# Kernel optimization log

Measured on AMD Instinct MI355X. Metric: run time of the kernel, lower is better.

## Reference

```python
import jax, jax.numpy as jnp
import numpy as np

EPS = 1e-5
N_HEADS = 16
D_NOPE = 128
D_ROPE = 64
D_QK = D_NOPE + D_ROPE  # 192
D_V = 128
KV_RANK = 512
SCALE = D_QK ** -0.5


def rms_norm(x, w, eps=EPS):
    return x * jax.lax.rsqrt(jnp.mean(x * x, axis=-1, keepdims=True) + eps) * w


def apply_rope(x, c, s):
    # x: [..., D_ROPE], c/s broadcastable [..., D_ROPE//2]; half-split rotation
    x0, x1 = x[..., : D_ROPE // 2], x[..., D_ROPE // 2 :]
    return jnp.concatenate([x0 * c - x1 * s, x0 * s + x1 * c], axis=-1)


def setup_inputs() -> dict:
    key = jax.random.key(0)
    ks = jax.random.split(key, 8)
    B, S, H_DIM = 2, 2048, 2048
    Q_RANK = 1536
    w = lambda k, shp: jax.random.normal(k, shp, dtype=jnp.float32) * 0.02
    # real RoPE tables: [max_seq, D_ROPE//2]
    inv_freq = 1.0 / (10000.0 ** (np.arange(0, D_ROPE, 2, dtype=np.float32) / D_ROPE))
    ang = np.arange(S, dtype=np.float32)[:, None] * inv_freq[None, :]
    return {
        "x": jax.random.normal(ks[0], (B, S, H_DIM), dtype=jnp.float32),
        "positions": jnp.arange(S, dtype=jnp.int64),
        "Wqa": w(ks[1], (H_DIM, Q_RANK)),
        "g_qa": jnp.ones((Q_RANK,), jnp.float32),
        "Wqb": w(ks[2], (Q_RANK, N_HEADS * D_QK)),
        "Wkva": w(ks[3], (H_DIM, KV_RANK + D_ROPE)),
        "g_kva": jnp.ones((KV_RANK,), jnp.float32),
        "Wkvb": w(ks[4], (KV_RANK, N_HEADS * (D_NOPE + D_V))),
        "Wo": w(ks[5], (N_HEADS * D_V, H_DIM)),
        "cos": jnp.asarray(np.cos(ang)),
        "sin": jnp.asarray(np.sin(ang)),
    }


def reference(x, positions, Wqa, g_qa, Wqb, Wkva, g_kva, Wkvb, Wo, cos, sin):
    B, S, _ = x.shape
    # Q path: low-rank down, RMSNorm, up
    q = rms_norm(x @ Wqa, g_qa) @ Wqb  # [B,S,H*D_QK]
    q = q.reshape(B, S, N_HEADS, D_QK)
    q_nope, q_rope = q[..., :D_NOPE], q[..., D_NOPE:]
    c = cos[positions]  # [S, D_ROPE//2]
    s = sin[positions]
    q_rope = apply_rope(q_rope, c[None, :, None, :], s[None, :, None, :])
    # KV path: joint down-proj, split latent / rope-key
    kv_a = x @ Wkva  # [B,S,KV_RANK+D_ROPE]
    kv_latent = rms_norm(kv_a[..., :KV_RANK], g_kva)
    k_rope = apply_rope(kv_a[..., KV_RANK:], c[None, :, :], s[None, :, :])  # [B,S,D_ROPE]
    # up-project latent to per-head k_nope and v
    kv_b = (kv_latent @ Wkvb).reshape(B, S, N_HEADS, D_NOPE + D_V)
    k_nope, v = kv_b[..., :D_NOPE], kv_b[..., D_NOPE:]
    k = jnp.concatenate(
        [k_nope, jnp.broadcast_to(k_rope[:, :, None, :], (B, S, N_HEADS, D_ROPE))], axis=-1
    )  # [B,S,H,D_QK]
    q_full = jnp.concatenate([q_nope, q_rope], axis=-1)  # [B,S,H,D_QK]
    # causal SDPA with d_qk != d_v
    scores = jnp.einsum("bqhd,bkhd->bhqk", q_full, k) * SCALE
    causal = jnp.tril(jnp.ones((S, S), dtype=bool))
    scores = jnp.where(causal[None, None, :, :], scores, -jnp.inf)
    p = jax.nn.softmax(scores, axis=-1)
    out = jnp.einsum("bhqk,bkhd->bqhd", p, v).reshape(B, S, N_HEADS * D_V)
    return out @ Wo
```

## Files before the change

### kernel.cpp

```cpp
#include <hip/hip_runtime.h>
#include <hip/hip_bf16.h>

typedef __bf16 bf16;
typedef __bf16 bf16x8 __attribute__((ext_vector_type(8)));
typedef __bf16 bf16x4 __attribute__((ext_vector_type(4)));
typedef float f32x4 __attribute__((ext_vector_type(4)));

#define B_    2
#define S_    2048
#define HD    2048
#define NH    16
#define DQK   192
#define DV    128
#define QR    1536
#define KVR   512
#define NTOK  4096
#define NKVB  4096
#define NQB   3072
#define NQKVA 2176

#define EXP2F(x) __builtin_amdgcn_exp2f(x)

static __device__ __forceinline__ void gload16(const void* g, void* l) {
  __builtin_amdgcn_global_load_lds(
      (const __attribute__((address_space(1))) void*)g,
      (__attribute__((address_space(3))) void*)l, 16, 0, 0);
}

__global__ __launch_bounds__(256) void cvt_bf16(const float* __restrict__ in,
                                                bf16* __restrict__ out, long n) {
  long i = ((long)blockIdx.x * 256 + threadIdx.x) * 4;
  if (i + 3 < n) {
    float4 v = *(const float4*)(in + i);
    bf16x4 o = {(bf16)v.x, (bf16)v.y, (bf16)v.z, (bf16)v.w};
    *(bf16x4*)(out + i) = o;
  }
}

struct TransArgs {
  const float *s0, *s1, *s2, *s3, *s4;
  bf16 *d0, *d1, *d2, *d3, *d4;
};
__global__ __launch_bounds__(256) void transpose_all(TransArgs a) {
  __shared__ float tile[32][33];
  int bid = blockIdx.x;
  int seg, rel;
  if      (bid < 3072)  { seg = 0; rel = bid; }
  else if (bid < 4352)  { seg = 1; rel = bid - 3072; }
  else if (bid < 8960)  { seg = 2; rel = bid - 4352; }
  else if (bid < 11008) { seg = 3; rel = bid - 8960; }
  else                  { seg = 4; rel = bid - 11008; }
  const float* in = seg == 0 ? a.s0 : seg == 1 ? a.s1 : seg == 2 ? a.s2 : seg == 3 ? a.s3 : a.s4;
  bf16* out       = seg == 0 ? a.d0 : seg == 1 ? a.d1 : seg == 2 ? a.d2 : seg == 3 ? a.d3 : a.d4;
  int R   = seg == 0 ? 2048 : seg == 1 ? 2048 : seg == 2 ? 1536 : seg == 3 ? 512 : 2048;
  int C   = seg == 0 ? 1536 : seg == 1 ? 576  : seg == 2 ? 3072 : seg == 3 ? 4096 : 2048;
  int Np  = seg == 0 ? 1536 : seg == 1 ? 640  : seg == 2 ? 3072 : seg == 3 ? 4096 : 2048;
  int nbx = seg == 0 ? 48   : seg == 1 ? 20   : seg == 2 ? 96   : seg == 3 ? 128 : 64;
  int c0 = (rel % nbx) * 32;
  int r0 = (rel / nbx) * 32;
  int tx = threadIdx.x & 31, ty = threadIdx.x >> 5;
#pragma unroll
  for (int i = 0; i < 4; ++i) {
    int r = r0 + ty + i * 8, c = c0 + tx;
    tile[ty + i * 8][tx] = (c < C) ? in[(long)r * C + c] : 0.f;
  }
  __syncthreads();
#pragma unroll
  for (int i = 0; i < 4; ++i) {
    int oc = c0 + ty + i * 8;
    if (oc < Np) out[(long)oc * R + r0 + tx] = (bf16)tile[tx][ty + i * 8];
  }
}

#define GEMM_CORE(A, Bt, K)                                                    \
  __shared__ bf16 As[128 * 64];                                                \
  __shared__ bf16 Bs[128 * 64];                                                \
  const int t = threadIdx.x;                                                   \
  const int l = t & 63;                                                        \
  const int w = t >> 6;                                                        \
  const int m0 = blockIdx.y * 128;                                             \
  const int n0 = blockIdx.x * 128;                                             \
  const int wr = (w >> 1) * 64;                                                \
  const int wc = (w & 1) * 64;                                                 \
  const int lr = l & 15;                                                       \
  const int lg = l >> 4;                                                       \
  f32x4 acc[4][4] = {};                                                        \
  for (int k0 = 0; k0 < (K); k0 += 64) {                                       \
    __syncthreads();                                                           \
    _Pragma("unroll")                                                          \
    for (int j = 0; j < 4; ++j) {                                              \
      int s = j * 256 + t;                                                     \
      int row = s >> 3, sc = s & 7;                                            \
      int c = sc ^ (row & 7);                                                  \
      gload16((A) + (long)(m0 + row) * (K) + k0 + c * 8,                       \
              As + (j * 256 + w * 64) * 8);                                    \
      gload16((Bt) + (long)(n0 + row) * (K) + k0 + c * 8,                      \
              Bs + (j * 256 + w * 64) * 8);                                    \
    }                                                                          \
    __syncthreads();                                                           \
    _Pragma("unroll")                                                          \
    for (int kh = 0; kh < 2; ++kh) {                                           \
      bf16x8 af[4], bfr[4];                                                    \
      _Pragma("unroll")                                                        \
      for (int m = 0; m < 4; ++m) {                                            \
        int row = wr + m * 16 + lr;                                            \
        af[m] = *(const bf16x8*)(As + row * 64 + (((kh * 4 + lg) ^ (row & 7)) << 3)); \
      }                                                                        \
      _Pragma("unroll")                                                        \
      for (int n = 0; n < 4; ++n) {                                            \
        int row = wc + n * 16 + lr;                                            \
        bfr[n] = *(const bf16x8*)(Bs + row * 64 + (((kh * 4 + lg) ^ (row & 7)) << 3)); \
      }                                                                        \
      _Pragma("unroll")                                                        \
      for (int m = 0; m < 4; ++m)                                              \
        _Pragma("unroll")                                                      \
        for (int n = 0; n < 4; ++n)                                            \
          acc[m][n] = __builtin_amdgcn_mfma_f32_16x16x32_bf16(af[m], bfr[n], acc[m][n], 0, 0, 0); \
    }                                                                          \
  }

template <typename CT>
__global__ __launch_bounds__(256) void gemm_bf16(const bf16* __restrict__ A,
                                                 const bf16* __restrict__ Bt,
                                                 CT* __restrict__ C,
                                                 int M, int N, int K) {
  GEMM_CORE(A, Bt, K)
#pragma unroll
  for (int m = 0; m < 4; ++m)
#pragma unroll
    for (int n = 0; n < 4; ++n)
#pragma unroll
      for (int v = 0; v < 4; ++v) {
        int row = m0 + wr + m * 16 + lg * 4 + v;
        int col = n0 + wc + n * 16 + lr;
        C[(long)row * N + col] = (CT)acc[m][n][v];
      }
}

#define G8P_CORE(A, Bt, K)                                                     \
  __shared__ bf16 As_[2][256 * 64];                                            \
  __shared__ bf16 Bs_[2][256 * 64];                                            \
  const int t = threadIdx.x;                                                   \
  const int w = t >> 6, l = t & 63;                                            \
  const int lr = l & 15, lg = l >> 4;                                          \
  const int wm = w >> 2, wn = w & 3;                                           \
  const int m0 = blockIdx.y * 256, n0 = blockIdx.x * 256;                      \
  const int NT = (K) >> 6;                                                     \
  const int tr = t >> 3, sc = t & 7;                                           \
  f32x4 acc[8][4] = {};                                                        \
  auto stg = [&](int kt, int j) {                                              \
    int jj = j & 3;                                                            \
    int row = jj * 64 + tr;                                                    \
    int c = sc ^ (row & 7);                                                    \
    const bf16* src = (j < 4)                                                  \
        ? (A)  + (long)(m0 + row) * (K) + kt * 64 + c * 8                      \
        : (Bt) + (long)(n0 + row) * (K) + kt * 64 + c * 8;                     \
    bf16* dst = ((j < 4) ? As_[kt & 1] : Bs_[kt & 1]) + (jj * 512 + w * 64) * 8; \
    gload16(src, dst);                                                         \
  };                                                                           \
  _Pragma("unroll") for (int j = 0; j < 8; ++j) stg(0, j);                     \
  _Pragma("unroll") for (int j = 0; j < 8; ++j) stg(1, j);                     \
  for (int kt = 0; kt < NT; ++kt) {                                            \
    const bf16* Ab = As_[kt & 1];                                              \
    const bf16* Bb = Bs_[kt & 1];                                              \
    if (kt == NT - 1) { asm volatile("s_waitcnt vmcnt(0)" ::: "memory"); }     \
    else              { asm volatile("s_waitcnt vmcnt(8)" ::: "memory"); }     \
    __builtin_amdgcn_s_barrier();                                              \
    asm volatile("" ::: "memory");                                             \
    bf16x8 af[8][2], bfr[4][2];                                                \
    _Pragma("unroll")                                                          \
    for (int mi = 0; mi < 8; ++mi) {                                           \
      int row = wm * 128 + mi * 16 + lr;                                       \
      _Pragma("unroll")                                                        \
      for (int kh = 0; kh < 2; ++kh)                                           \
        af[mi][kh] = *(const bf16x8*)(Ab + row * 64 + (((kh * 4 + lg) ^ (row & 7)) << 3)); \
    }                                                                          \
    _Pragma("unroll")                                                          \
    for (int ni = 0; ni < 4; ++ni) {                                           \
      int row = wn * 64 + ni * 16 + lr;                                        \
      _Pragma("unroll")                                                        \
      for (int kh = 0; kh < 2; ++kh)                                           \
        bfr[ni][kh] = *(const bf16x8*)(Bb + row * 64 + (((kh * 4 + lg) ^ (row & 7)) << 3)); \
    }                                                                          \
    asm volatile("s_waitcnt lgkmcnt(0)" ::: "memory");                         \
    __builtin_amdgcn_sched_barrier(0);                                         \
    __builtin_amdgcn_s_setprio(1);                                             \
    _Pragma("unroll")                                                          \
    for (int mi = 0; mi < 8; ++mi)                                             \
      _Pragma("unroll")                                                        \
      for (int kh = 0; kh < 2; ++kh)                                           \
        acc[mi][0] = __builtin_amdgcn_mfma_f32_16x16x32_bf16(af[mi][kh], bfr[0][kh], acc[mi][0], 0, 0, 0); \
    __builtin_amdgcn_s_setprio(0);                                             \
    __builtin_amdgcn_s_barrier();    \
    asm volatile("" ::: "memory");                                             \
    bool more = (kt + 2) < NT;                                                 \
    if (more) { stg(kt + 2, 0); stg(kt + 2, 1); stg(kt + 2, 2); }              \
    __builtin_amdgcn_s_setprio(1);                                             \
    _Pragma("unroll")                                                          \
    for (int mi = 0; mi < 8; ++mi)                                             \
      _Pragma("unroll")                                                        \
      for (int kh = 0; kh < 2; ++kh)                                           \
        acc[mi][1] = __builtin_amdgcn_mfma_f32_16x16x32_bf16(af[mi][kh], bfr[1][kh], acc[mi][1], 0, 0, 0); \
    __builtin_amdgcn_s_setprio(0);                                             \
    if (more) { stg(kt + 2, 3); stg(kt + 2, 4); stg(kt + 2, 5); }              \
    __builtin_amdgcn_s_setprio(1);                                             \
    _Pragma("unroll")                                                          \
    for (int mi = 0; mi < 8; ++mi)                                             \
      _Pragma("unroll")                                                        \
      for (int kh = 0; kh < 2; ++kh)                                           \
        acc[mi][2] = __builtin_amdgcn_mfma_f32_16x16x32_bf16(af[mi][kh], bfr[2][kh], acc[mi][2], 0, 0, 0); \
    __builtin_amdgcn_s_setprio(0);                                             \
    if (more) { stg(kt + 2, 6); stg(kt + 2, 7); }                              \
    __builtin_amdgcn_s_setprio(1);                                             \
    _Pragma("unroll")                                                          \
    for (int mi = 0; mi < 8; ++mi)                                             \
      _Pragma("unroll")                                                        \
      for (int kh = 0; kh < 2; ++kh)                                           \
        acc[mi][3] = __builtin_amdgcn_mfma_f32_16x16x32_bf16(af[mi][kh], bfr[3][kh], acc[mi][3], 0, 0, 0); \
    __builtin_amdgcn_s_setprio(0);                                             \
  }

__global__ __launch_bounds__(512) void gemm8p_qf(const bf16* __restrict__ A,
                                                 const bf16* __restrict__ Bt,
                                                 const int* __restrict__ pos,
                                                 const float* __restrict__ cosT,
                                                 const float* __restrict__ sinT,
                                                 bf16* __restrict__ q_bhsd) {
  const float SCALE = 0.07216878364870323f * 1.4426950408889634f;
  G8P_CORE(A, Bt, QR)
  int c0 = n0 + wn * 64;
  int h = c0 / 192;
  int part = c0 - h * 192;
#pragma unroll
  for (int mi = 0; mi < 8; ++mi)
#pragma unroll
    for (int v = 0; v < 4; ++v) {
      int row = m0 + wm * 128 + mi * 16 + lg * 4 + v;
      int b = row >> 11, s = row & (S_ - 1);
      long base = ((long)(b * NH + h) * S_ + s) * DQK;
      if (part < 128) {
#pragma unroll
        for (int ni = 0; ni < 4; ++ni)
          q_bhsd[base + part + ni * 16 + lr] = (bf16)(acc[mi][ni][v] * SCALE);
      } else {
        int p = pos[s] & (S_ - 1);
        float c_lo = cosT[p * 32 + lr],      s_lo = sinT[p * 32 + lr];
        float c_hi = cosT[p * 32 + 16 + lr], s_hi = sinT[p * 32 + 16 + lr];
        float o0 = acc[mi][0][v] * c_lo - acc[mi][2][v] * s_lo;
        float o1 = acc[mi][1][v] * c_hi - acc[mi][3][v] * s_hi;
        float o2 = acc[mi][0][v] * s_lo + acc[mi][2][v] * c_lo;
        float o3 = acc[mi][1][v] * s_hi + acc[mi][3][v] * c_hi;
        q_bhsd[base + 128 + lr] = (bf16)(o0 * SCALE);
        q_bhsd[base + 144 + lr] = (bf16)(o1 * SCALE);
        q_bhsd[base + 160 + lr] = (bf16)(o2 * SCALE);
        q_bhsd[base + 176 + lr] = (bf16)(o3 * SCALE);
      }
    }
}

__global__ __launch_bounds__(512) void gemm8p_kvb(const bf16* __restrict__ A,
                                                  const bf16* __restrict__ Bt,
                                                  bf16* __restrict__ k_bhsd,
                                                  bf16* __restrict__ v_t) {
  G8P_CORE(A, Bt, KVR)
  int c0 = n0 + wn * 64;
  int h = c0 >> 8;
  int dbase = c0 & 64;
  bool vpart = (c0 >> 7) & 1;
  if (!vpart) {
#pragma unroll
    for (int mi = 0; mi < 8; ++mi)
#pragma unroll
      for (int v = 0; v < 4; ++v) {
        int row = m0 + wm * 128 + mi * 16 + lg * 4 + v;
        int b = row >> 11, s = row & (S_ - 1);
        long base = ((long)(b * NH + h) * S_ + s) * DQK + dbase;
#pragma unroll
        for (int ni = 0; ni < 4; ++ni)
          k_bhsd[base + ni * 16 + lr] = (bf16)acc[mi][ni][v];
      }
  } else {
#pragma unroll
    for (int mi = 0; mi < 8; ++mi) {
      int row0 = m0 + wm * 128 + mi * 16 + lg * 4;
      int b = row0 >> 11, s = row0 & (S_ - 1);
#pragma unroll
      for (int ni = 0; ni < 4; ++ni) {
        int d = dbase + ni * 16 + lr;
        bf16x4 o = {(bf16)acc[mi][ni][0], (bf16)acc[mi][ni][1],
                    (bf16)acc[mi][ni][2], (bf16)acc[mi][ni][3]};
        *(bf16x4*)(v_t + ((long)(b * NH + h) * DV + d) * S_ + s) = o;
      }
    }
  }
}

__global__ __launch_bounds__(256) void norm_prep(const bf16* __restrict__ xa,
                                                 const float* __restrict__ g_qa,
                                                 const float* __restrict__ g_kva,
                                                 const int* __restrict__ pos,
                                                 const float* __restrict__ cosT,
                                                 const float* __restrict__ sinT,
                                                 bf16* __restrict__ q_n,
                                                 bf16* __restrict__ kv_l,
                                                 bf16* __restrict__ k_bhsd) {
  int row = blockIdx.x;
  int t = threadIdx.x;
  int b = row >> 11, s = row & (S_ - 1);
  const bf16* xr = xa + (long)row * NQKVA;
  __shared__ float red[3];
  __shared__ bf16 rope_s[64];
  float vf[8];
  if (t < 192) {
    bf16x8 vv = *(const bf16x8*)(xr + t * 8);
    float ss = 0.f;
#pragma unroll
    for (int e = 0; e < 8; ++e) { vf[e] = (float)vv[e]; ss += vf[e] * vf[e]; }
#pragma unroll
    for (int m = 1; m < 64; m <<= 1) ss += __shfl_xor(ss, m);
    if ((t & 63) == 0) red[t >> 6] = ss;
  } else {
    int tt = t - 192;
    const bf16* xl = xr + QR;
    bf16x8 vv = *(const bf16x8*)(xl + tt * 8);
    float ss = 0.f;
#pragma unroll
    for (int e = 0; e < 8; ++e) { vf[e] = (float)vv[e]; ss += vf[e] * vf[e]; }
#pragma unroll
    for (int m = 1; m < 64; m <<= 1) ss += __shfl_xor(ss, m);
    float rs = rsqrtf(ss / KVR + 1e-5f);
    bf16x8 o;
#pragma unroll
    for (int e = 0; e < 8; ++e) o[e] = (bf16)(vf[e] * rs * g_kva[tt * 8 + e]);
    *(bf16x8*)(kv_l + (long)row * KVR + tt * 8) = o;
    if (tt < 32) {
      int p = pos[s] & (S_ - 1);
      float c = cosT[p * 32 + tt], sn = sinT[p * 32 + tt];
      float x0 = (float)xl[512 + tt], x1 = (float)xl[544 + tt];
      rope_s[tt] = (bf16)(x0 * c - x1 * sn);
      rope_s[32 + tt] = (bf16)(x0 * sn + x1 * c);
    }
  }
  __syncthreads();
  if (t < 192) {
    float ss = red[0] + red[1] + red[2];
    float rs = rsqrtf(ss / QR + 1e-5f);
    bf16x8 o;
#pragma unroll
    for (int e = 0; e < 8; ++e) o[e] = (bf16)(vf[e] * rs * g_qa[t * 8 + e]);
    *(bf16x8*)(q_n + (long)row * QR + t * 8) = o;
  } else {
    int tt = t - 192;
    bf16x8 rv = *(const bf16x8*)&rope_s[(tt & 7) * 8];
    long base0 = ((long)(b * NH + (tt >> 3)) * S_ + s) * DQK + 128 + (tt & 7) * 8;
    long base1 = ((long)(b * NH + 8 + (tt >> 3)) * S_ + s) * DQK + 128 + (tt & 7) * 8;
    *(bf16x8*)(k_bhsd + base0) = rv;
    *(bf16x8*)(k_bhsd + base1) = rv;
  }
}

#define KVB  64
#define DVP  144
__global__ __launch_bounds__(512) void flash4(const bf16* __restrict__ q_bhsd,
                                              const bf16* __restrict__ k_bhsd,
                                              const bf16* __restrict__ v_t,
                                              bf16* __restrict__ att) {
  __shared__ bf16 Ks[KVB * DQK];
  __shared__ bf16 Vs[DVP * KVB];
  __shared__ bf16 Ps[8][16 * 72];
  int bid = blockIdx.x;
  int bh = bid & 31;
  int qt = 15 - (bid >> 5);
  int b = bh >> 4, h = bh & 15;
  int q0 = qt * 128;
  int t = threadIdx.x;
  int w = t >> 6, l = t & 63;
  int lr = l & 15, lg = l >> 4;
  int qw = q0 + w * 16;

  const bf16* Qb = q_bhsd + (long)bh * S_ * DQK;
  const bf16* Kb = k_bhsd + (long)bh * S_ * DQK;
  const bf16* Vb = v_t + (long)bh * DV * S_;

  if (t < 128) {
    int rr = 128 + (t >> 3), cc = (t & 7) * 8;
    bf16 val = (bf16)((rr == 128) ? 1.0f : 0.0f);
    bf16x8 vvv = {val, val, val, val, val, val, val, val};
    *(bf16x8*)(Vs + rr * KVB + cc) = vvv;
  }

  bf16x8 qf[6];
#pragma unroll
  for (int t6 = 0; t6 < 6; ++t6)
    qf[t6] = *(const bf16x8*)(Qb + (long)(qw + lr) * DQK + t6 * 32 + lg * 8);

  f32x4 oacc[9] = {};
  float mrow[4] = {-1e30f, -1e30f, -1e30f, -1e30f};
  const int lr7 = lr & 7;

  int nkt = 2 * qt + 2;
  for (int kt = 0; kt < nkt; ++kt) {
    int k0 = kt * KVB;
    __syncthreads();
#pragma unroll
    for (int j = 0; j < 3; ++j) {
      int s = j * 512 + t;
      int r = s / 24, c1 = s - r * 24;
      int c = c1 ^ (r & 7);
      gload16(Kb + (long)(k0 + r) * DQK + c * 8, Ks + (j * 512 + w * 64) * 8);
    }
#pragma unroll
    for (int j = 0; j < 2; ++j) {
      int s = j * 512 + t;
      int d = s >> 3, c1 = s & 7;
      int c = c1 ^ (d & 7);
      gload16(Vb + (long)d * S_ + k0 + c * 8, Vs + (j * 512 + w * 64) * 8);
    }
    __syncthreads();
    if (k0 > qw + 15) continue;

    f32x4 sacc[4] = {};
#pragma unroll
    for (int n = 0; n < 4; ++n) {
      int rk = n * 16 + lr;
#pragma unroll
      for (int t6 = 0; t6 < 6; ++t6) {
        bf16x8 kf = *(const bf16x8*)(Ks + rk * DQK + (((t6 * 4 + lg) ^ lr7) << 3));
        sacc[n] = __builtin_amdgcn_mfma_f32_16x16x32_bf16(qf[t6], kf, sacc[n], 0, 0, 0);
      }
    }
    if (k0 + KVB - 1 > qw) {
#pragma unroll
      for (int n = 0; n < 4; ++n)
#pragma unroll
        for (int v = 0; v < 4; ++v) {
          int r = lg * 4 + v, c = n * 16 + lr;
          if (k0 + c > qw + r) sacc[n][v] = -1e30f;
        }
    }
    float mv[4];
#pragma unroll
    for (int v = 0; v < 4; ++v) {
      mv[v] = fmaxf(fmaxf(sacc[0][v], sacc[1][v]), fmaxf(sacc[2][v], sacc[3][v]));
#pragma unroll
      for (int msk = 1; msk < 16; msk <<= 1) mv[v] = fmaxf(mv[v], __shfl_xor(mv[v], msk));
    }
    bool grow = (mv[0] > mrow[0] + 8.f) | (mv[1] > mrow[1] + 8.f) |
                (mv[2] > mrow[2] + 8.f) | (mv[3] > mrow[3] + 8.f);
    if (__any(grow)) {
      float corr[4];
#pragma unroll
      for (int v = 0; v < 4; ++v) {
        float mt = fmaxf(mrow[v], mv[v]);
        corr[v] = EXP2F(mrow[v] - mt);
        mrow[v] = mt;
      }
#pragma unroll
      for (int dn = 0; dn < 9; ++dn)
#pragma unroll
        for (int v = 0; v < 4; ++v) oacc[dn][v] *= corr[v];
    }
#pragma unroll
    for (int v = 0; v < 4; ++v)
#pragma unroll
      for (int n = 0; n < 4; ++n)
        Ps[w][(lg * 4 + v) * 72 + n * 16 + lr] = (bf16)EXP2F(sacc[n][v] - mrow[v]);
#pragma unroll
    for (int kc = 0; kc < 2; ++kc) {
      bf16x8 pf = *(const bf16x8*)(Ps[w] + lr * 72 + kc * 32 + lg * 8);
#pragma unroll
      for (int dn = 0; dn < 9; ++dn) {
        int d = dn * 16 + lr;
        bf16x8 vf = *(const bf16x8*)(Vs + d * KVB + (((kc * 4 + lg) ^ lr7) << 3));
        oacc[dn] = __builtin_amdgcn_mfma_f32_16x16x32_bf16(pf, vf, oacc[dn], 0, 0, 0);
      }
    }
  }
  float rl[4];
#pragma unroll
  for (int v = 0; v < 4; ++v) {
    float lv = __shfl(oacc[8][v], lg * 16);
    rl[v] = 1.0f / lv;
  }
#pragma unroll
  for (int dn = 0; dn < 8; ++dn)
#pragma unroll
    for (int v = 0; v < 4; ++v) {
      int r = lg * 4 + v;
      float o = oacc[dn][v] * rl[v];
      att[((long)(b * S_ + qw + r)) * 2048 + h * 128 + dn * 16 + lr] = (bf16)o;
    }
}

extern "C" void kernel_launch(void* const* d_in, const int* in_sizes, int n_in,
                              void* d_out, int out_size, void* d_ws, size_t ws_size,
                              hipStream_t stream) {
  const float* x        = (const float*)d_in[0];
  const int* pos        = (const int*)d_in[1];
  const float* Wqa      = (const float*)d_in[2];
  const float* g_qa     = (const float*)d_in[3];
  const float* Wqb      = (const float*)d_in[4];
  const float* Wkva     = (const float*)d_in[5];
  const float* g_kva    = (const float*)d_in[6];
  const float* Wkvb     = (const float*)d_in[7];
  const float* Wo       = (const float*)d_in[8];
  const float* cosT     = (const float*)d_in[9];
  const float* sinT     = (const float*)d_in[10];
  float* out            = (float*)d_out;

  size_t off = 0;
  char* wsp = (char*)d_ws;
  auto alloc = [&](size_t n) { void* p = wsp + off; off += (n + 255) & ~(size_t)255; return p; };
  bf16*  Wqa_t  = (bf16*) alloc((size_t)QR * HD * 2);
  bf16*  Wkva_t = (bf16*) alloc((size_t)640 * HD * 2);
  bf16*  Wqb_t  = (bf16*) alloc((size_t)NQB * QR * 2);
  bf16*  Wkvb_t = (bf16*) alloc((size_t)NKVB * KVR * 2);
  bf16*  Wo_t   = (bf16*) alloc((size_t)HD * HD * 2);
  bf16*  x_bf   = (bf16*) alloc((size_t)NTOK * HD * 2);
  bf16*  q_bhsd = (bf16*) alloc((size_t)B_ * NH * S_ * DQK * 2);
  bf16*  k_bhsd = (bf16*) alloc((size_t)B_ * NH * S_ * DQK * 2);
  bf16*  v_t    = (bf16*) alloc((size_t)B_ * NH * DV * S_ * 2);
  bf16*  att    = (bf16*) alloc((size_t)NTOK * 2048 * 2);
  char*  T      = (char*) alloc((size_t)33554432);
  bf16*  xa  = (bf16*)T;
  bf16*  q_n = (bf16*)(T + 18874368);
  bf16*  kv_l = (bf16*)(T + 18874368 + 12582912);
  if (ws_size < off) return;

  cvt_bf16<<<(NTOK * HD / 4 + 255) / 256, 256, 0, stream>>>(x, x_bf, (long)NTOK * HD);
  TransArgs ta = {Wqa, Wkva, Wqb, Wkvb, Wo, Wqa_t, Wkva_t, Wqb_t, Wkvb_t, Wo_t};
  transpose_all<<<15104, 256, 0, stream>>>(ta);
  gemm_bf16<bf16><<<dim3(NQKVA / 128, NTOK / 128), 256, 0, stream>>>(x_bf, Wqa_t, xa, NTOK, NQKVA, HD);
  norm_prep<<<NTOK, 256, 0, stream>>>(xa, g_qa, g_kva, pos, cosT, sinT, q_n, kv_l, k_bhsd);
  gemm8p_qf<<<dim3(NQB / 256, NTOK / 256), 512, 0, stream>>>(q_n, Wqb_t, pos, cosT, sinT, q_bhsd);
  gemm8p_kvb<<<dim3(NKVB / 256, NTOK / 256), 512, 0, stream>>>(kv_l, Wkvb_t, k_bhsd, v_t);
  flash4<<<512, 512, 0, stream>>>(q_bhsd, k_bhsd, v_t, att);
  gemm_bf16<float><<<dim3(HD / 128, NTOK / 128), 256, 0, stream>>>(att, Wo_t, out, NTOK, HD, HD);
}
```

Baseline: 298.1 us.

## Double-buffer K/V tiles in flash attention to overlap loads with compute

```diff
diff --git a/kernel.cpp b/kernel.cpp
--- a/kernel.cpp
+++ b/kernel.cpp
@@ -360,13 +360,13 @@
 }
 
 #define KVB  64
-#define DVP  144
-__global__ __launch_bounds__(512) void flash4(const bf16* __restrict__ q_bhsd,
+__global__ __launch_bounds__(512) void flash5(const bf16* __restrict__ q_bhsd,
                                               const bf16* __restrict__ k_bhsd,
                                               const bf16* __restrict__ v_t,
                                               bf16* __restrict__ att) {
-  __shared__ bf16 Ks[KVB * DQK];
-  __shared__ bf16 Vs[DVP * KVB];
+  __shared__ bf16 Ks[2][KVB * DQK];
+  __shared__ bf16 Vs[2][DV * KVB];
+  __shared__ bf16 Vones[16 * KVB];
   __shared__ bf16 Ps[8][16 * 72];
   int bid = blockIdx.x;
   int bh = bid & 31;
@@ -377,16 +377,17 @@
   int w = t >> 6, l = t & 63;
   int lr = l & 15, lg = l >> 4;
   int qw = q0 + w * 16;
+  const int lr7 = lr & 7;
 
   const bf16* Qb = q_bhsd + (long)bh * S_ * DQK;
   const bf16* Kb = k_bhsd + (long)bh * S_ * DQK;
   const bf16* Vb = v_t + (long)bh * DV * S_;
 
   if (t < 128) {
-    int rr = 128 + (t >> 3), cc = (t & 7) * 8;
-    bf16 val = (bf16)((rr == 128) ? 1.0f : 0.0f);
+    int rr = t >> 3, cc = (t & 7) * 8;
+    bf16 val = (bf16)((rr == 0) ? 1.0f : 0.0f);
     bf16x8 vvv = {val, val, val, val, val, val, val, val};
-    *(bf16x8*)(Vs + rr * KVB + cc) = vvv;
+    *(bf16x8*)(Vones + rr * KVB + cc) = vvv;
   }
 
   bf16x8 qf[6];
@@ -396,85 +397,102 @@
 
   f32x4 oacc[9] = {};
   float mrow[4] = {-1e30f, -1e30f, -1e30f, -1e30f};
-  const int lr7 = lr & 7;
 
   int nkt = 2 * qt + 2;
+
+#define STAGE5(kt)                                                            \
+  {                                                                           \
+    int k0_ = (kt) * KVB;                                                     \
+    _Pragma("unroll")                                                         \
+    for (int j = 0; j < 3; ++j) {                                             \
+      int s_ = j * 512 + t;                                                   \
+      int r_ = s_ / 24, c1_ = s_ - r_ * 24;                                   \
+      int c_ = c1_ ^ (r_ & 7);                                                \
+      gload16(Kb + (long)(k0_ + r_) * DQK + c_ * 8,                           \
+              Ks[(kt) & 1] + (j * 512 + w * 64) * 8);                         \
+    }                                                                         \
+    _Pragma("unroll")                                                         \
+    for (int j = 0; j < 2; ++j) {                                             \
+      int s_ = j * 512 + t;                                                   \
+      int d_ = s_ >> 3, c1_ = s_ & 7;                                         \
+      int c_ = c1_ ^ (d_ & 7);                                                \
+      gload16(Vb + (long)d_ * S_ + k0_ + c_ * 8,                              \
+              Vs[(kt) & 1] + (j * 512 + w * 64) * 8);                         \
+    }                                                                         \
+  }
+
+  STAGE5(0)
   for (int kt = 0; kt < nkt; ++kt) {
+    if (kt + 1 < nkt) {
+      STAGE5(kt + 1)
+      asm volatile("s_waitcnt vmcnt(5)" ::: "memory");
+    } else {
+      asm volatile("s_waitcnt vmcnt(0)" ::: "memory");
+    }
+    __builtin_amdgcn_s_barrier();
     int k0 = kt * KVB;
-    __syncthreads();
-#pragma unroll
-    for (int j = 0; j < 3; ++j) {
-      int s = j * 512 + t;
-      int r = s / 24, c1 = s - r * 24;
-      int c = c1 ^ (r & 7);
-      gload16(Kb + (long)(k0 + r) * DQK + c * 8, Ks + (j * 512 + w * 64) * 8);
+    if (k0 <= qw + 15) {
+      const bf16* Kc = Ks[kt & 1];
+      const bf16* Vc = Vs[kt & 1];
+      f32x4 sacc[4] = {};
+#pragma unroll
+      for (int n = 0; n < 4; ++n) {
+        int rk = n * 16 + lr;
+#pragma unroll
+        for (int t6 = 0; t6 < 6; ++t6) {
+          bf16x8 kf = *(const bf16x8*)(Kc + rk * DQK + (((t6 * 4 + lg) ^ lr7) << 3));
+          sacc[n] = __builtin_amdgcn_mfma_f32_16x16x32_bf16(qf[t6], kf, sacc[n], 0, 0, 0);
+        }
+      }
+      if (k0 + KVB - 1 > qw) {
+#pragma unroll
+        for (int n = 0; n < 4; ++n)
+#pragma unroll
+          for (int v = 0; v < 4; ++v) {
+            int r = lg * 4 + v, c = n * 16 + lr;
+            if (k0 + c > qw + r) sacc[n][v] = -1e30f;
+          }
+      }
+      float mv[4];
+#pragma unroll
+      for (int v = 0; v < 4; ++v) {
+        mv[v] = fmaxf(fmaxf(sacc[0][v], sacc[1][v]), fmaxf(sacc[2][v], sacc[3][v]));
+#pragma unroll
+        for (int msk = 1; msk < 16; msk <<= 1) mv[v] = fmaxf(mv[v], __shfl_xor(mv[v], msk));
+      }
+      bool grow = (mv[0] > mrow[0] + 8.f) | (mv[1] > mrow[1] + 8.f) |
+                  (mv[2] > mrow[2] + 8.f) | (mv[3] > mrow[3] + 8.f);
+      if (__any(grow)) {
+        float corr[4];
+#pragma unroll
+        for (int v = 0; v < 4; ++v) {
+          float mt = fmaxf(mrow[v], mv[v]);
+          corr[v] = EXP2F(mrow[v] - mt);
+          mrow[v] = mt;
+        }
+#pragma unroll
+        for (int dn = 0; dn < 9; ++dn)
+#pragma unroll
+          for (int v = 0; v < 4; ++v) oacc[dn][v] *= corr[v];
+      }
+#pragma unroll
+      for (int v = 0; v < 4; ++v)
+#pragma unroll
+        for (int n = 0; n < 4; ++n)
+          Ps[w][(lg * 4 + v) * 72 + n * 16 + lr] = (bf16)EXP2F(sacc[n][v] - mrow[v]);
+#pragma unroll
+      for (int kc = 0; kc < 2; ++kc) {
+        bf16x8 pf = *(const bf16x8*)(Ps[w] + lr * 72 + kc * 32 + lg * 8);
+#pragma unroll
+        for (int dn = 0; dn < 9; ++dn) {
+          const bf16* vb = (dn < 8) ? (Vc + (dn * 16 + lr) * KVB)
+                                    : (Vones + lr * KVB);
+          bf16x8 vf = *(const bf16x8*)(vb + (((kc * 4 + lg) ^ lr7) << 3));
+          oacc[dn] = __builtin_amdgcn_mfma_f32_16x16x32_bf16(pf, vf, oacc[dn], 0, 0, 0);
+        }
+      }
     }
-#pragma unroll
-    for (int j = 0; j < 2; ++j) {
-      int s = j * 512 + t;
-      int d = s >> 3, c1 = s & 7;
-      int c = c1 ^ (d & 7);
-      gload16(Vb + (long)d * S_ + k0 + c * 8, Vs + (j * 512 + w * 64) * 8);
-    }
-    __syncthreads();
-    if (k0 > qw + 15) continue;
-
-    f32x4 sacc[4] = {};
-#pragma unroll
-    for (int n = 0; n < 4; ++n) {
-      int rk = n * 16 + lr;
-#pragma unroll
-      for (int t6 = 0; t6 < 6; ++t6) {
-        bf16x8 kf = *(const bf16x8*)(Ks + rk * DQK + (((t6 * 4 + lg) ^ lr7) << 3));
-        sacc[n] = __builtin_amdgcn_mfma_f32_16x16x32_bf16(qf[t6], kf, sacc[n], 0, 0, 0);
-      }
-    }
-    if (k0 + KVB - 1 > qw) {
-#pragma unroll
-      for (int n = 0; n < 4; ++n)
-#pragma unroll
-        for (int v = 0; v < 4; ++v) {
-          int r = lg * 4 + v, c = n * 16 + lr;
-          if (k0 + c > qw + r) sacc[n][v] = -1e30f;
-        }
-    }
-    float mv[4];
-#pragma unroll
-    for (int v = 0; v < 4; ++v) {
-      mv[v] = fmaxf(fmaxf(sacc[0][v], sacc[1][v]), fmaxf(sacc[2][v], sacc[3][v]));
-#pragma unroll
-      for (int msk = 1; msk < 16; msk <<= 1) mv[v] = fmaxf(mv[v], __shfl_xor(mv[v], msk));
-    }
-    bool grow = (mv[0] > mrow[0] + 8.f) | (mv[1] > mrow[1] + 8.f) |
-                (mv[2] > mrow[2] + 8.f) | (mv[3] > mrow[3] + 8.f);
-    if (__any(grow)) {
-      float corr[4];
-#pragma unroll
-      for (int v = 0; v < 4; ++v) {
-        float mt = fmaxf(mrow[v], mv[v]);
-        corr[v] = EXP2F(mrow[v] - mt);
-        mrow[v] = mt;
-      }
-#pragma unroll
-      for (int dn = 0; dn < 9; ++dn)
-#pragma unroll
-        for (int v = 0; v < 4; ++v) oacc[dn][v] *= corr[v];
-    }
-#pragma unroll
-    for (int v = 0; v < 4; ++v)
-#pragma unroll
-      for (int n = 0; n < 4; ++n)
-        Ps[w][(lg * 4 + v) * 72 + n * 16 + lr] = (bf16)EXP2F(sacc[n][v] - mrow[v]);
-#pragma unroll
-    for (int kc = 0; kc < 2; ++kc) {
-      bf16x8 pf = *(const bf16x8*)(Ps[w] + lr * 72 + kc * 32 + lg * 8);
-#pragma unroll
-      for (int dn = 0; dn < 9; ++dn) {
-        int d = dn * 16 + lr;
-        bf16x8 vf = *(const bf16x8*)(Vs + d * KVB + (((kc * 4 + lg) ^ lr7) << 3));
-        oacc[dn] = __builtin_amdgcn_mfma_f32_16x16x32_bf16(pf, vf, oacc[dn], 0, 0, 0);
-      }
-    }
+    __builtin_amdgcn_s_barrier();
   }
   float rl[4];
 #pragma unroll
@@ -534,6 +552,6 @@
   norm_prep<<<NTOK, 256, 0, stream>>>(xa, g_qa, g_kva, pos, cosT, sinT, q_n, kv_l, k_bhsd);
   gemm8p_qf<<<dim3(NQB / 256, NTOK / 256), 512, 0, stream>>>(q_n, Wqb_t, pos, cosT, sinT, q_bhsd);
   gemm8p_kvb<<<dim3(NKVB / 256, NTOK / 256), 512, 0, stream>>>(kv_l, Wkvb_t, k_bhsd, v_t);
-  flash4<<<512, 512, 0, stream>>>(q_bhsd, k_bhsd, v_t, att);
+  flash5<<<512, 512, 0, stream>>>(q_bhsd, k_bhsd, v_t, att);
   gemm_bf16<float><<<dim3(HD / 128, NTOK / 128), 256, 0, stream>>>(att, Wo_t, out, NTOK, HD, HD);
 }
```

Measured after the change: 298.6 us. About the same (+0.2%).

## Give each flash-attention wave 32 query rows to reuse K/V fragments

Applied to the files above, without the earlier changes.

```diff
diff --git a/kernel.cpp b/kernel.cpp
--- a/kernel.cpp
+++ b/kernel.cpp
@@ -361,13 +361,13 @@
 
 #define KVB  64
 #define DVP  144
-__global__ __launch_bounds__(512) void flash4(const bf16* __restrict__ q_bhsd,
+__global__ __launch_bounds__(256) void flash6(const bf16* __restrict__ q_bhsd,
                                               const bf16* __restrict__ k_bhsd,
                                               const bf16* __restrict__ v_t,
                                               bf16* __restrict__ att) {
   __shared__ bf16 Ks[KVB * DQK];
   __shared__ bf16 Vs[DVP * KVB];
-  __shared__ bf16 Ps[8][16 * 72];
+  __shared__ bf16 Ps[4][32 * 72];
   int bid = blockIdx.x;
   int bh = bid & 31;
   int qt = 15 - (bid >> 5);
@@ -376,7 +376,8 @@
   int t = threadIdx.x;
   int w = t >> 6, l = t & 63;
   int lr = l & 15, lg = l >> 4;
-  int qw = q0 + w * 16;
+  int qw = q0 + w * 32;
+  const int lr7 = lr & 7;
 
   const bf16* Qb = q_bhsd + (long)bh * S_ * DQK;
   const bf16* Kb = k_bhsd + (long)bh * S_ * DQK;
@@ -389,107 +390,129 @@
     *(bf16x8*)(Vs + rr * KVB + cc) = vvv;
   }
 
-  bf16x8 qf[6];
-#pragma unroll
-  for (int t6 = 0; t6 < 6; ++t6)
-    qf[t6] = *(const bf16x8*)(Qb + (long)(qw + lr) * DQK + t6 * 32 + lg * 8);
-
-  f32x4 oacc[9] = {};
-  float mrow[4] = {-1e30f, -1e30f, -1e30f, -1e30f};
-  const int lr7 = lr & 7;
+  bf16x8 qf[2][6];
+#pragma unroll
+  for (int rg = 0; rg < 2; ++rg)
+#pragma unroll
+    for (int t6 = 0; t6 < 6; ++t6)
+      qf[rg][t6] = *(const bf16x8*)(Qb + (long)(qw + rg * 16 + lr) * DQK + t6 * 32 + lg * 8);
+
+  f32x4 oacc[2][9] = {};
+  float mrow[2][4] = {{-1e30f,-1e30f,-1e30f,-1e30f},{-1e30f,-1e30f,-1e30f,-1e30f}};
 
   int nkt = 2 * qt + 2;
   for (int kt = 0; kt < nkt; ++kt) {
     int k0 = kt * KVB;
     __syncthreads();
 #pragma unroll
-    for (int j = 0; j < 3; ++j) {
-      int s = j * 512 + t;
+    for (int j = 0; j < 6; ++j) {
+      int s = j * 256 + t;
       int r = s / 24, c1 = s - r * 24;
       int c = c1 ^ (r & 7);
-      gload16(Kb + (long)(k0 + r) * DQK + c * 8, Ks + (j * 512 + w * 64) * 8);
-    }
-#pragma unroll
-    for (int j = 0; j < 2; ++j) {
-      int s = j * 512 + t;
+      gload16(Kb + (long)(k0 + r) * DQK + c * 8, Ks + (j * 256 + w * 64) * 8);
+    }
+#pragma unroll
+    for (int j = 0; j < 4; ++j) {
+      int s = j * 256 + t;
       int d = s >> 3, c1 = s & 7;
       int c = c1 ^ (d & 7);
-      gload16(Vb + (long)d * S_ + k0 + c * 8, Vs + (j * 512 + w * 64) * 8);
+      gload16(Vb + (long)d * S_ + k0 + c * 8, Vs + (j * 256 + w * 64) * 8);
     }
     __syncthreads();
-    if (k0 > qw + 15) continue;
-
-    f32x4 sacc[4] = {};
+    if (k0 > qw + 31) continue;
+
+    f32x4 sacc[2][4] = {};
 #pragma unroll
     for (int n = 0; n < 4; ++n) {
       int rk = n * 16 + lr;
 #pragma unroll
       for (int t6 = 0; t6 < 6; ++t6) {
         bf16x8 kf = *(const bf16x8*)(Ks + rk * DQK + (((t6 * 4 + lg) ^ lr7) << 3));
-        sacc[n] = __builtin_amdgcn_mfma_f32_16x16x32_bf16(qf[t6], kf, sacc[n], 0, 0, 0);
+        sacc[0][n] = __builtin_amdgcn_mfma_f32_16x16x32_bf16(qf[0][t6], kf, sacc[0][n], 0, 0, 0);
+        sacc[1][n] = __builtin_amdgcn_mfma_f32_16x16x32_bf16(qf[1][t6], kf, sacc[1][n], 0, 0, 0);
       }
     }
     if (k0 + KVB - 1 > qw) {
 #pragma unroll
-      for (int n = 0; n < 4; ++n)
+      for (int rg = 0; rg < 2; ++rg)
+#pragma unroll
+        for (int n = 0; n < 4; ++n)
+#pragma unroll
+          for (int v = 0; v < 4; ++v) {
+            int r = rg * 16 + lg * 4 + v, c = n * 16 + lr;
+            if (k0 + c > qw + r) sacc[rg][n][v] = -1e30f;
+          }
+    }
+    float mv[2][4];
+#pragma unroll
+    for (int rg = 0; rg < 2; ++rg)
+#pragma unroll
+      for (int v = 0; v < 4; ++v) {
+        mv[rg][v] = fmaxf(fmaxf(sacc[rg][0][v], sacc[rg][1][v]),
+                          fmaxf(sacc[rg][2][v], sacc[rg][3][v]));
+#pragma unroll
+        for (int msk = 1; msk < 16; msk <<= 1)
+          mv[rg][v] = fmaxf(mv[rg][v], __shfl_xor(mv[rg][v], msk));
+      }
+    bool grow = false;
+#pragma unroll
+    for (int rg = 0; rg < 2; ++rg)
+#pragma unroll
+      for (int v = 0; v < 4; ++v) grow |= (mv[rg][v] > mrow[rg][v] + 8.f);
+    if (__any(grow)) {
+#pragma unroll
+      for (int rg = 0; rg < 2; ++rg) {
+        float corr[4];
 #pragma unroll
         for (int v = 0; v < 4; ++v) {
-          int r = lg * 4 + v, c = n * 16 + lr;
-          if (k0 + c > qw + r) sacc[n][v] = -1e30f;
+          float mt = fmaxf(mrow[rg][v], mv[rg][v]);
+          corr[v] = EXP2F(mrow[rg][v] - mt);
+          mrow[rg][v] = mt;
         }
-    }
-    float mv[4];
-#pragma unroll
-    for (int v = 0; v < 4; ++v) {
-      mv[v] = fmaxf(fmaxf(sacc[0][v], sacc[1][v]), fmaxf(sacc[2][v], sacc[3][v]));
-#pragma unroll
-      for (int msk = 1; msk < 16; msk <<= 1) mv[v] = fmaxf(mv[v], __shfl_xor(mv[v], msk));
-    }
-    bool grow = (mv[0] > mrow[0] + 8.f) | (mv[1] > mrow[1] + 8.f) |
-                (mv[2] > mrow[2] + 8.f) | (mv[3] > mrow[3] + 8.f);
-    if (__any(grow)) {
-      float corr[4];
-#pragma unroll
-      for (int v = 0; v < 4; ++v) {
-        float mt = fmaxf(mrow[v], mv[v]);
-        corr[v] = EXP2F(mrow[v] - mt);
-        mrow[v] = mt;
-      }
-#pragma unroll
-      for (int dn = 0; dn < 9; ++dn)
-#pragma unroll
-        for (int v = 0; v < 4; ++v) oacc[dn][v] *= corr[v];
-    }
-#pragma unroll
-    for (int v = 0; v < 4; ++v)
-#pragma unroll
-      for (int n = 0; n < 4; ++n)
-        Ps[w][(lg * 4 + v) * 72 + n * 16 + lr] = (bf16)EXP2F(sacc[n][v] - mrow[v]);
+#pragma unroll
+        for (int dn = 0; dn < 9; ++dn)
+#pragma unroll
+          for (int v = 0; v < 4; ++v) oacc[rg][dn][v] *= corr[v];
+      }
+    }
+#pragma unroll
+    for (int rg = 0; rg < 2; ++rg)
+#pragma unroll
+      for (int v = 0; v < 4; ++v)
+#pragma unroll
+        for (int n = 0; n < 4; ++n)
+          Ps[w][(rg * 16 + lg * 4 + v) * 72 + n * 16 + lr] =
+              (bf16)EXP2F(sacc[rg][n][v] - mrow[rg][v]);
 #pragma unroll
     for (int kc = 0; kc < 2; ++kc) {
-      bf16x8 pf = *(const bf16x8*)(Ps[w] + lr * 72 + kc * 32 + lg * 8);
+      bf16x8 pf0 = *(const bf16x8*)(Ps[w] + lr * 72 + kc * 32 + lg * 8);
+      bf16x8 pf1 = *(const bf16x8*)(Ps[w] + (16 + lr) * 72 + kc * 32 + lg * 8);
 #pragma unroll
       for (int dn = 0; dn < 9; ++dn) {
         int d = dn * 16 + lr;
         bf16x8 vf = *(const bf16x8*)(Vs + d * KVB + (((kc * 4 + lg) ^ lr7) << 3));
-        oacc[dn] = __builtin_amdgcn_mfma_f32_16x16x32_bf16(pf, vf, oacc[dn], 0, 0, 0);
-      }
-    }
-  }
-  float rl[4];
-#pragma unroll
-  for (int v = 0; v < 4; ++v) {
-    float lv = __shfl(oacc[8][v], lg * 16);
-    rl[v] = 1.0f / lv;
-  }
-#pragma unroll
-  for (int dn = 0; dn < 8; ++dn)
+        oacc[0][dn] = __builtin_amdgcn_mfma_f32_16x16x32_bf16(pf0, vf, oacc[0][dn], 0, 0, 0);
+        oacc[1][dn] = __builtin_amdgcn_mfma_f32_16x16x32_bf16(pf1, vf, oacc[1][dn], 0, 0, 0);
+      }
+    }
+  }
+#pragma unroll
+  for (int rg = 0; rg < 2; ++rg) {
+    float rl[4];
 #pragma unroll
     for (int v = 0; v < 4; ++v) {
-      int r = lg * 4 + v;
-      float o = oacc[dn][v] * rl[v];
-      att[((long)(b * S_ + qw + r)) * 2048 + h * 128 + dn * 16 + lr] = (bf16)o;
-    }
+      float lv = __shfl(oacc[rg][8][v], lg * 16);
+      rl[v] = 1.0f / lv;
+    }
+#pragma unroll
+    for (int dn = 0; dn < 8; ++dn)
+#pragma unroll
+      for (int v = 0; v < 4; ++v) {
+        int r = rg * 16 + lg * 4 + v;
+        float o = oacc[rg][dn][v] * rl[v];
+        att[((long)(b * S_ + qw + r)) * 2048 + h * 128 + dn * 16 + lr] = (bf16)o;
+      }
+  }
 }
 
 extern "C" void kernel_launch(void* const* d_in, const int* in_sizes, int n_in,
@@ -534,6 +557,6 @@
   norm_prep<<<NTOK, 256, 0, stream>>>(xa, g_qa, g_kva, pos, cosT, sinT, q_n, kv_l, k_bhsd);
   gemm8p_qf<<<dim3(NQB / 256, NTOK / 256), 512, 0, stream>>>(q_n, Wqb_t, pos, cosT, sinT, q_bhsd);
   gemm8p_kvb<<<dim3(NKVB / 256, NTOK / 256), 512, 0, stream>>>(kv_l, Wkvb_t, k_bhsd, v_t);
-  flash4<<<512, 512, 0, stream>>>(q_bhsd, k_bhsd, v_t, att);
+  flash6<<<512, 256, 0, stream>>>(q_bhsd, k_bhsd, v_t, att);
   gemm_bf16<float><<<dim3(HD / 128, NTOK / 128), 256, 0, stream>>>(att, Wo_t, out, NTOK, HD, HD);
 }
```

New measurement: 320.9 us. 1.08x slower.
